# Performance work log

Hardware: AMD Instinct MI355X
Metric: run time of the kernel (lower is better)

## Reference

```python
import jax, jax.numpy as jnp
import numpy as np

B, N, IN, HID, OUT = 64, 256, 7, 64, 32
DEG = 32
NT = B * N          # total nodes per side
E = NT * DEG        # intra-graph edges per side
TAU = 1.0
MAX_ITER = 10
EPS = 1e-5          # InstanceNorm2d eps


def setup_inputs() -> dict:
    key = jax.random.key(0)
    ks = jax.random.split(key, 12)

    def edges(k):
        # random intra-graph edges: local indices in [0, N) plus per-graph offset
        loc = jax.random.randint(k, (2, B, N * DEG), 0, N)
        off = (jnp.arange(B) * N)[None, :, None]
        return (loc + off).reshape(2, -1).astype(jnp.int64)

    def lin(k, fi, fo):
        return jax.random.normal(k, (fi, fo), jnp.float32) / np.float32(np.sqrt(fi))

    return {
        "x1": jax.random.normal(ks[0], (NT, IN), jnp.float32),
        "x2": jax.random.normal(ks[1], (NT, IN), jnp.float32),
        "edge1": edges(ks[2]),
        "edge2": edges(ks[3]),
        "Wl1": lin(ks[4], IN, HID), "Wr1": lin(ks[5], IN, HID),
        "bl1": jnp.zeros((HID,), jnp.float32), "br1": jnp.zeros((HID,), jnp.float32),
        "att1": jax.random.normal(ks[6], (HID,), jnp.float32) * 0.1,
        "bias1": jnp.zeros((HID,), jnp.float32),
        "Wl2": lin(ks[7], HID, OUT), "Wr2": lin(ks[8], HID, OUT),
        "bl2": jnp.zeros((OUT,), jnp.float32), "br2": jnp.zeros((OUT,), jnp.float32),
        "att2": jax.random.normal(ks[9], (OUT,), jnp.float32) * 0.1,
        "bias2": jnp.zeros((OUT,), jnp.float32),
        "gamma": jnp.ones((1,), jnp.float32),
        "beta": jnp.zeros((1,), jnp.float32),
    }


def _gatv2(x, src, dst, Wl, bl, Wr, br, att, bias):
    # PyG GATv2Conv, heads=1: score = att . leaky_relu(lin_l(x_j) + lin_r(x_i))
    xl = x @ Wl + bl  # source transform
    xr = x @ Wr + br  # target transform
    e = jax.nn.leaky_relu(xl[src] + xr[dst], 0.2)     # [E, D]
    score = e @ att                                    # [E]
    smax = jax.ops.segment_max(score, dst, num_segments=NT)
    ex = jnp.exp(score - smax[dst])
    den = jax.ops.segment_sum(ex, dst, num_segments=NT)
    alpha = ex / den[dst]
    out = jax.ops.segment_sum(alpha[:, None] * xl[src], dst, num_segments=NT)
    return out + bias


def _encode(x, edge, params):
    # add self loops (PyG add_self_loops=True default)
    loops = jnp.arange(NT)
    src = jnp.concatenate([edge[0], loops])
    dst = jnp.concatenate([edge[1], loops])
    h = jax.nn.relu(_gatv2(x, src, dst, *params[0]))
    return _gatv2(h, src, dst, *params[1])


def _soft_topk(sim_n):
    # AFAT-style differentiable top-k: OT between flattened scores and
    # {min, max} anchors with marginals [(n-k)/n, k/n], k = N2 per pair.
    n = N * N
    k = N
    flat = sim_n.reshape(B, n)
    mn = flat.min(axis=1, keepdims=True)
    mx = flat.max(axis=1, keepdims=True)
    dist = jnp.stack([flat - mn, mx - flat], axis=-1)  # [B, n, 2] (|s-min|,|s-max|)
    logK = -dist / TAU
    log_row = -jnp.log(jnp.float32(n))
    log_col = jnp.log(jnp.array([(n - k) / n, k / n], jnp.float32))
    for i in range(MAX_ITER):
        if i % 2 == 0:  # row normalization to uniform 1/n
            logK = logK - jax.scipy.special.logsumexp(logK, axis=-1, keepdims=True) + log_row
        else:           # column normalization to [(n-k)/n, k/n]
            logK = logK - jax.scipy.special.logsumexp(logK, axis=1, keepdims=True) + log_col[None, None, :]
    soft = jnp.clip(jnp.exp(logK[:, :, 1]) * n, 0.0, 1.0)  # selection probability per entry
    return soft.reshape(B, N, N)


def reference(x1, x2, edge1, edge2, Wl1, Wr1, bl1, br1, att1, bias1,
              Wl2, Wr2, bl2, br2, att2, bias2, gamma, beta):
    params = ((Wl1, bl1, Wr1, br1, att1, bias1), (Wl2, bl2, Wr2, br2, att2, bias2))
    h1 = _encode(x1, edge1, params).reshape(B, N, OUT)
    h2 = _encode(x2, edge2, params).reshape(B, N, OUT)
    sim = jnp.einsum('bnd,bmd->bnm', h1, h2)
    # InstanceNorm2d(1, affine=True): normalize each pair's sim matrix
    mu = sim.mean(axis=(1, 2), keepdims=True)
    var = sim.var(axis=(1, 2), keepdims=True)
    sim_n = gamma[0] * (sim - mu) * jax.lax.rsqrt(var + EPS) + beta[0]
    return _soft_topk(sim_n)  # soft_S stacked over the batch, [B, N, N]
```

## Files before the change

### kernel.cpp

```cpp
#include <hip/hip_runtime.h>

#define NB 64
#define NN 256
#define IND 7
#define HIDD 64
#define OUTD 32
#define EPG 8192
#define ETOT 524288
#define CAPQ 2600
#define SRCPAD 2624

typedef _Float16 f16;
typedef f16 f16x2 __attribute__((ext_vector_type(2)));
typedef f16 f16x4 __attribute__((ext_vector_type(4)));
typedef f16 f16x8 __attribute__((ext_vector_type(8)));
typedef float f32x4 __attribute__((ext_vector_type(4)));

__device__ __forceinline__ float bsum16(float v, float* rb){
#pragma unroll
  for (int o = 32; o > 0; o >>= 1) v += __shfl_xor(v, o, 64);
  __syncthreads();
  if ((threadIdx.x & 63) == 0) rb[threadIdx.x >> 6] = v;
  __syncthreads();
  float s = 0.f;
#pragma unroll
  for (int i = 0; i < 16; i++) s += rb[i];
  return s;
}

__device__ __forceinline__ f16x2 lrelu2(f16x2 s){
  const f16x2 k = {(f16)0.2f, (f16)0.2f};
  return __builtin_elementwise_max(s, s * k);
}

__global__ __launch_bounds__(512, 4) void gat1(
    const float* __restrict__ x1, const float* __restrict__ x2,
    const int* __restrict__ e1, const int* __restrict__ e2,
    const float* __restrict__ Wl, const float* __restrict__ Wr,
    const float* __restrict__ bl, const float* __restrict__ br,
    const float* __restrict__ att, const float* __restrict__ bias,
    const float* __restrict__ Wl2, const float* __restrict__ Wr2,
    const float* __restrict__ bl2, const float* __restrict__ br2,
    f16* __restrict__ xl2, f16* __restrict__ xr2,
    int* __restrict__ meta, unsigned char* __restrict__ srcs)
{
  __shared__ __align__(16) f16 xl_s[256 * 72];
  __shared__ __align__(16) f16 xr1_s[64 * 72];
  __shared__ __align__(16) f16 att_s[64];
  __shared__ float sc_s[CAPQ + 8];
  __shared__ unsigned int src_su[SRCPAD / 4];
  __shared__ int deg_s[64], start_s[64], cnt_s[64];
  __shared__ unsigned char perm[64];
  unsigned char* src_s = (unsigned char*)src_su;

  const int bid = blockIdx.x;
  const int gs = bid & 127, lo = (bid >> 7) * 64;
  const int side = gs >> 6, g = gs & 63;
  const float* x = side ? x2 : x1;
  const int* eb = side ? e2 : e1;
  const int* es = eb + g * EPG;
  const int* ed = eb + ETOT + g * EPG;
  const int t = threadIdx.x;
  const int wv = t >> 6, lane64 = t & 63;

  if (t < 64){ deg_s[t] = 0; att_s[t] = (f16)att[t]; }

  unsigned int ep2[9];
  int nE = 0;
#pragma unroll
  for (int i = 0; i < 17; i++){
    int e = t + i * 512;
    if (e < EPG + 256){
      int sl, dl;
      if (e < EPG){ sl = es[e] & 255; dl = ed[e] & 255; }
      else { sl = dl = e - EPG; }
      unsigned int pk = (unsigned int)((dl << 8) | sl);
      if ((i & 1) == 0) ep2[i >> 1] = pk;
      else ep2[i >> 1] |= pk << 16;
      nE = i + 1;
    }
  }

  float xvl[IND], xvr[IND];
  {
    const int nodel = (wv & 3) * 64 + lane64;
    const float* pl = x + (g * 256 + nodel) * IND;
    const float* pr = x + (g * 256 + lo + lane64) * IND;
#pragma unroll
    for (int k = 0; k < IND; k++){ xvl[k] = pl[k]; xvr[k] = pr[k]; }
  }
  __syncthreads();

#pragma unroll
  for (int i = 0; i < 17; i++) if (i < nE){
    unsigned int pk = (ep2[i >> 1] >> (16 * (i & 1))) & 0xFFFFu;
    int r = (int)(pk >> 8) - lo;
    if ((unsigned)r < 64u) atomicAdd(&deg_s[r], 1);
  }
  __syncthreads();
  if (t < 64){
    int v = deg_s[t], s = v;
#pragma unroll
    for (int off = 1; off < 64; off <<= 1){
      int u = __shfl_up(s, off, 64);
      if (t >= off) s += u;
    }
    start_s[t] = s - v;
    cnt_s[t] = s - v;
    meta[bid * 128 + t] = s - v;
    meta[bid * 128 + 64 + t] = v;
    int r = 0;
#pragma unroll 8
    for (int j = 0; j < 64; j++){
      int dj = deg_s[j];
      r += (dj < v) || (dj == v && j < t);
    }
    perm[r] = (unsigned char)t;
  }
  __syncthreads();
#pragma unroll
  for (int i = 0; i < 17; i++) if (i < nE){
    unsigned int pk = (ep2[i >> 1] >> (16 * (i & 1))) & 0xFFFFu;
    int r = (int)(pk >> 8) - lo;
    if ((unsigned)r < 64u){
      int p = atomicAdd(&cnt_s[r], 1);
      if (p < CAPQ) src_s[p] = (unsigned char)(pk & 255u);
    }
  }
  __syncthreads();
  {
    int ttl = start_s[63] + deg_s[63];
    if (ttl > CAPQ) ttl = CAPQ;
    unsigned int* gsrc = (unsigned int*)(srcs + (size_t)bid * SRCPAD);
    int nw = (ttl + 3) >> 2;
    for (int i = t; i < nw; i += 512) gsrc[i] = src_su[i];
  }

  {
    const int ng = wv & 3, dh = wv >> 2;
    const int node = ng * 64 + lane64;
#pragma unroll
    for (int ch = 0; ch < 4; ch++){
      const int d0 = dh * 32 + ch * 8;
      float a[8];
#pragma unroll
      for (int d = 0; d < 8; d++) a[d] = bl[d0 + d];
#pragma unroll
      for (int k = 0; k < IND; k++){
        float xk = xvl[k];
#pragma unroll
        for (int d = 0; d < 8; d++)
          a[d] = fmaf(xk, Wl[k * HIDD + d0 + d], a[d]);
      }
      f16x8 o;
#pragma unroll
      for (int j = 0; j < 8; j++) o[j] = (f16)a[j];
      *(f16x8*)&xl_s[node * 72 + d0] = o;
    }
  }
  {
    const int d0 = wv * 8;
    float a[8];
#pragma unroll
    for (int d = 0; d < 8; d++) a[d] = br[d0 + d];
#pragma unroll
    for (int k = 0; k < IND; k++){
      float xk = xvr[k];
#pragma unroll
      for (int d = 0; d < 8; d++)
        a[d] = fmaf(xk, Wr[k * HIDD + d0 + d], a[d]);
    }
    f16x8 o;
#pragma unroll
    for (int j = 0; j < 8; j++) o[j] = (f16)a[j];
    *(f16x8*)&xr1_s[lane64 * 72 + d0] = o;
  }
  __syncthreads();

  const int pairi = perm[t >> 3], sub = t & 7, ln = lo + pairi;
  f16x2 xrh[32], atth[32];
  {
    const f16x8* xrp = (const f16x8*)&xr1_s[pairi * 72];
    const f16x8* atp = (const f16x8*)att_s;
#pragma unroll
    for (int q = 0; q < 8; q++){
      f16x8 v = xrp[q], a_ = atp[q];
#pragma unroll
      for (int u = 0; u < 4; u++){
        xrh[q * 4 + u][0] = v[2 * u];
        xrh[q * 4 + u][1] = v[2 * u + 1];
        atth[q * 4 + u][0] = a_[2 * u];
        atth[q * 4 + u][1] = a_[2 * u + 1];
      }
    }
  }

  const int s0 = start_s[pairi];
  int sE = s0 + deg_s[pairi];
  if (sE > CAPQ) sE = CAPQ;
  float ssum = 0.f;
  for (int idx = s0 + sub; idx < sE; idx += 8){
    int sl = src_s[idx];
    const f16x8* rp = (const f16x8*)&xl_s[(unsigned)sl * 72];
    float accs[4] = {0.f, 0.f, 0.f, 0.f};
#pragma unroll
    for (int blk = 0; blk < 8; blk++){
      f16x8 rv = rp[blk];
#pragma unroll
      for (int u = 0; u < 4; u++){
        f16x2 v = {rv[2 * u], rv[2 * u + 1]};
        v = v + xrh[blk * 4 + u];
        accs[u] = __builtin_amdgcn_fdot2(lrelu2(v), atth[blk * 4 + u], accs[u], false);
      }
    }
    float w = __expf((accs[0] + accs[1]) + (accs[2] + accs[3]));
    sc_s[idx] = w;
    ssum += w;
  }
  ssum += __shfl_xor(ssum, 1, 64);
  ssum += __shfl_xor(ssum, 2, 64);
  ssum += __shfl_xor(ssum, 4, 64);
  float inv = 1.f / ssum;
  float acc[8];
#pragma unroll
  for (int c = 0; c < 8; c++) acc[c] = 0.f;
  for (int base = s0; base < sE; base += 4){
    f16x8 rows[4]; float wv_[4];
#pragma unroll
    for (int k = 0; k < 4; k++){
      int sl = src_s[base + k];
      rows[k] = *(const f16x8*)&xl_s[(unsigned)sl * 72 + sub * 8];
      wv_[k] = sc_s[base + k];
    }
#pragma unroll
    for (int k = 0; k < 4; k++){
      float w = (base + k < sE) ? wv_[k] : 0.f;
#pragma unroll
      for (int c = 0; c < 8; c++) acc[c] = fmaf(w, (float)rows[k][c], acc[c]);
    }
  }
  f16x8 o;
#pragma unroll
  for (int c = 0; c < 8; c++)
    o[c] = (f16)fmaxf(acc[c] * inv + bias[sub * 8 + c], 0.f);

  __syncthreads();
  *(f16x8*)&xl_s[pairi * 72 + sub * 8] = o;
  __syncthreads();
  if (wv < 4){
    const int m = lane64 & 15, quad = lane64 >> 4;
    const int row = wv * 16 + m;
    f16x8 a0 = *(const f16x8*)&xl_s[row * 72 + quad * 8];
    f16x8 a1 = *(const f16x8*)&xl_s[row * 72 + 32 + quad * 8];
#pragma unroll
    for (int mat = 0; mat < 2; mat++){
      const float* W = mat ? Wr2 : Wl2;
      const float* bb = mat ? br2 : bl2;
      f16* dst = mat ? xr2 : xl2;
#pragma unroll
      for (int H = 0; H < 2; H++){
        const int n = H * 16 + m;
        f16x8 b0, b1;
#pragma unroll
        for (int j = 0; j < 8; j++){
          b0[j] = (f16)W[(quad * 8 + j) * 32 + n];
          b1[j] = (f16)W[(32 + quad * 8 + j) * 32 + n];
        }
        const float bv = bb[n];
        f32x4 accm = {0.f, 0.f, 0.f, 0.f};
        accm = __builtin_amdgcn_mfma_f32_16x16x32_f16(a0, b0, accm, 0, 0, 0);
        accm = __builtin_amdgcn_mfma_f32_16x16x32_f16(a1, b1, accm, 0, 0, 0);
#pragma unroll
        for (int r = 0; r < 4; r++)
          dst[(size_t)(gs * 256 + lo + wv * 16 + quad * 4 + r) * 32 + n]
              = (f16)(accm[r] + bv);
      }
    }
  }
}

__global__ __launch_bounds__(512, 4) void gat2(
    const int* __restrict__ meta, const unsigned char* __restrict__ srcs,
    const f16* __restrict__ xl2, const f16* __restrict__ xr2,
    const float* __restrict__ att, const float* __restrict__ bias,
    f16* __restrict__ hout)
{
  __shared__ __align__(16) f16 xl_s[256 * 40];
  __shared__ __align__(16) f16 xr_s[64 * 40];
  __shared__ float sc_s[CAPQ + 8];
  __shared__ unsigned int src_su[SRCPAD / 4];
  __shared__ int start_s[64], deg_s[64];
  __shared__ unsigned char perm[64];
  unsigned char* src_s = (unsigned char*)src_su;

  const int bid = blockIdx.x;
  const int gs = bid & 127, lo = (bid >> 7) * 64;
  const int t = threadIdx.x;

  if (t < 64){
    start_s[t] = meta[bid * 128 + t];
    deg_s[t] = meta[bid * 128 + 64 + t];
  }
  {
    int ttl = meta[bid * 128 + 63] + meta[bid * 128 + 64 + 63];
    if (ttl > CAPQ) ttl = CAPQ;
    const unsigned int* gsrc = (const unsigned int*)(srcs + (size_t)bid * SRCPAD);
    int nw = (ttl + 3) >> 2;
    for (int i = t; i < nw; i += 512) src_su[i] = gsrc[i];
  }

  {
    const int row = t >> 1, half = t & 1;
    const f16* s_ = xl2 + (size_t)(gs * 256 + row) * 32 + half * 16;
    *(f16x8*)&xl_s[row * 40 + half * 16] = *(const f16x8*)s_;
    *(f16x8*)&xl_s[row * 40 + half * 16 + 8] = *(const f16x8*)(s_ + 8);
    if (t < 128){
      const f16* s2_ = xr2 + (size_t)(gs * 256 + lo + row) * 32 + half * 16;
      *(f16x8*)&xr_s[row * 40 + half * 16] = *(const f16x8*)s2_;
      *(f16x8*)&xr_s[row * 40 + half * 16 + 8] = *(const f16x8*)(s2_ + 8);
    }
  }
  __syncthreads();
  if (t < 64){
    int v = deg_s[t], r = 0;
#pragma unroll 8
    for (int j = 0; j < 64; j++){
      int dj = deg_s[j];
      r += (dj < v) || (dj == v && j < t);
    }
    perm[r] = (unsigned char)t;
  }
  __syncthreads();

  const int pairi = perm[t >> 3], sub = t & 7, ln = lo + pairi;
  f16x2 xrh[16], atth[16];
  {
    const f16x8* xrp = (const f16x8*)&xr_s[pairi * 40];
#pragma unroll
    for (int q = 0; q < 4; q++){
      f16x8 v = xrp[q];
#pragma unroll
      for (int u = 0; u < 4; u++){
        xrh[q * 4 + u][0] = v[2 * u];
        xrh[q * 4 + u][1] = v[2 * u + 1];
      }
    }
#pragma unroll
    for (int i = 0; i < 16; i++){
      atth[i][0] = (f16)att[2 * i];
      atth[i][1] = (f16)att[2 * i + 1];
    }
  }

  const int s0 = start_s[pairi];
  int sE = s0 + deg_s[pairi];
  if (sE > CAPQ) sE = CAPQ;
  float ssum = 0.f;
  for (int idx = s0 + sub; idx < sE; idx += 8){
    int sl = src_s[idx];
    const f16x8* rp = (const f16x8*)&xl_s[(unsigned)sl * 40];
    float accs[4] = {0.f, 0.f, 0.f, 0.f};
#pragma unroll
    for (int blk = 0; blk < 4; blk++){
      f16x8 rv = rp[blk];
#pragma unroll
      for (int u = 0; u < 4; u++){
        f16x2 v = {rv[2 * u], rv[2 * u + 1]};
        v = v + xrh[blk * 4 + u];
        accs[u] = __builtin_amdgcn_fdot2(lrelu2(v), atth[blk * 4 + u], accs[u], false);
      }
    }
    float w = __expf((accs[0] + accs[1]) + (accs[2] + accs[3]));
    sc_s[idx] = w;
    ssum += w;
  }
  ssum += __shfl_xor(ssum, 1, 64);
  ssum += __shfl_xor(ssum, 2, 64);
  ssum += __shfl_xor(ssum, 4, 64);
  float inv = 1.f / ssum;

  float acc[4];
#pragma unroll
  for (int c = 0; c < 4; c++) acc[c] = 0.f;
  for (int base = s0; base < sE; base += 8){
    f16x4 rows[8]; float wv[8];
#pragma unroll
    for (int k = 0; k < 8; k++){
      int sl = src_s[base + k];
      rows[k] = *(const f16x4*)&xl_s[(unsigned)sl * 40 + sub * 4];
      wv[k] = sc_s[base + k];
    }
#pragma unroll
    for (int k = 0; k < 8; k++){
      float w = (base + k < sE) ? wv[k] : 0.f;
#pragma unroll
      for (int c = 0; c < 4; c++) acc[c] = fmaf(w, (float)rows[k][c], acc[c]);
    }
  }
  f16x4 o;
#pragma unroll
  for (int c = 0; c < 4; c++)
    o[c] = (f16)(acc[c] * inv + bias[sub * 4 + c]);
  *(f16x4*)(hout + (size_t)(gs * 256 + ln) * 32 + sub * 4) = o;
}

__global__ __launch_bounds__(1024) void sinkout(
    const f16* __restrict__ H,
    const float* __restrict__ gamma, const float* __restrict__ beta,
    float* __restrict__ out)
{
  __shared__ float rb[16];
  __shared__ __align__(16) float rb4s[64];
  __shared__ unsigned int hist[8192];
  const int b = blockIdx.x & 63, q = blockIdx.x >> 6, t = threadIdx.x;
  const int w = t >> 6, lane = t & 63;
  const int m = lane & 15, quad = lane >> 4;

  const f16* h1 = H + (size_t)b * 256 * 32;
  const f16* h2 = H + (size_t)(64 + b) * 256 * 32;

  f16x8 av = *(const f16x8*)(h1 + (size_t)(w * 16 + m) * 32 + quad * 8);
  f32x4 c[16];
#pragma unroll
  for (int j = 0; j < 16; j++){
    f16x8 bv = *(const f16x8*)(h2 + (size_t)(j * 16 + m) * 32 + quad * 8);
    f32x4 z = {0.f, 0.f, 0.f, 0.f};
    c[j] = __builtin_amdgcn_mfma_f32_16x16x32_f16(av, bv, z, 0, 0, 0);
  }

  float sm = 0.f, s2 = 0.f, mn = 3.0e38f, mx = -3.0e38f;
#pragma unroll
  for (int j = 0; j < 16; j++)
#pragma unroll
    for (int r = 0; r < 4; r++){
      float s = c[j][r];
      sm += s; s2 = fmaf(s, s, s2);
      mn = fminf(mn, s); mx = fmaxf(mx, s);
    }
#pragma unroll
  for (int o = 32; o > 0; o >>= 1){
    sm += __shfl_xor(sm, o, 64);
    s2 += __shfl_xor(s2, o, 64);
    mn = fminf(mn, __shfl_xor(mn, o, 64));
    mx = fmaxf(mx, __shfl_xor(mx, o, 64));
  }
  if (lane == 0){
    rb4s[w * 4 + 0] = sm; rb4s[w * 4 + 1] = s2;
    rb4s[w * 4 + 2] = mn; rb4s[w * 4 + 3] = mx;
  }
  for (int i = t; i < 8192; i += 1024) hist[i] = 0u;
  __syncthreads();
  sm = 0.f; s2 = 0.f; mn = 3.0e38f; mx = -3.0e38f;
#pragma unroll
  for (int i = 0; i < 16; i++){
    sm += rb4s[i * 4 + 0];
    s2 += rb4s[i * 4 + 1];
    mn = fminf(mn, rb4s[i * 4 + 2]);
    mx = fmaxf(mx, rb4s[i * 4 + 3]);
  }

  const float mu = sm * (1.f / 65536.f);
  const float var = s2 * (1.f / 65536.f) - mu * mu;
  const float a = gamma[0] * rsqrtf(var + 1e-5f);
  const float cc = beta[0] - a * mu;
  float mnn = a * mn + cc, mxn = a * mx + cc;
  if (a < 0.f){ float tmp = mnn; mnn = mxn; mxn = tmp; }
  const float al = 2.f * a;
  const float be = 2.f * cc - mnn - mxn;
  const float R = fmaxf(mxn - mnn, 1e-12f);
  const float binscale = 4096.f / R;

#pragma unroll
  for (int j = 0; j < 16; j++)
#pragma unroll
    for (int r = 0; r < 4; r++){
      float z = fmaf(al, c[j][r], be);
      int bi = (int)fmaf(z, binscale, 4096.f);
      bi = min(max(bi, 0), 8191);
      atomicAdd(&hist[bi], 1u);
    }
  __syncthreads();

  const float wbin = R * (1.f / 4096.f);
  float ebs[8], cnts[8];
#pragma unroll
  for (int j = 0; j < 8; j++){
    float zc = fmaf((float)(t * 8 + j) + 0.5f, wbin, -R);
    ebs[j] = __expf(-zc);
    cnts[j] = (float)hist[t * 8 + j];
  }

  float D = 0.f, S = 256.f, eD = 1.f;
  for (int p = 0; p < 5; p++){
    float loc = 0.f;
#pragma unroll
    for (int j = 0; j < 8; j++)
      loc += cnts[j] / (1.f + ebs[j] * eD);
    S = bsum16(loc, rb);
    if (p < 4){
      D += -5.5412635f  + __logf(65536.f - S) - __logf(S);
      eD = __expf(-D);
    }
  }

  const float beD = be + D;
  const float scale = 256.f / S;
  if ((w >> 2) == q){
    float* ob = out + (size_t)b * 65536;
#pragma unroll
    for (int j = 0; j < 16; j++){
#pragma unroll
      for (int r = 0; r < 4; r++){
        float zz = fmaf(al, c[j][r], beD);
        float v = fminf(scale / (1.f + __expf(-zz)), 1.f);
        ob[(w * 16 + quad * 4 + r) * 256 + j * 16 + m] = v;
      }
    }
  }
}

extern "C" void kernel_launch(void* const* d_in, const int* in_sizes, int n_in,
                              void* d_out, int out_size, void* d_ws, size_t ws_size,
                              hipStream_t stream)
{
  const float* x1   = (const float*)d_in[0];
  const float* x2   = (const float*)d_in[1];
  const int*   e1   = (const int*)d_in[2];
  const int*   e2   = (const int*)d_in[3];
  const float* Wl1  = (const float*)d_in[4];
  const float* Wr1  = (const float*)d_in[5];
  const float* bl1  = (const float*)d_in[6];
  const float* br1  = (const float*)d_in[7];
  const float* att1 = (const float*)d_in[8];
  const float* bias1= (const float*)d_in[9];
  const float* Wl2  = (const float*)d_in[10];
  const float* Wr2  = (const float*)d_in[11];
  const float* bl2  = (const float*)d_in[12];
  const float* br2  = (const float*)d_in[13];
  const float* att2 = (const float*)d_in[14];
  const float* bias2= (const float*)d_in[15];
  const float* gamma= (const float*)d_in[16];
  const float* beta = (const float*)d_in[17];

  char* ws = (char*)d_ws;
  f16* hfin = (f16*)ws;
  f16* xl2 = (f16*)(ws + (size_t)2 * 1024 * 1024);
  f16* xr2 = (f16*)(ws + (size_t)4 * 1024 * 1024);
  int* meta = (int*)(ws + (size_t)6 * 1024 * 1024);
  unsigned char* srcs = (unsigned char*)(ws + (size_t)6 * 1024 * 1024 + 512 * 128 * 4);
  float* out = (float*)d_out;

  gat1<<<512, 512, 0, stream>>>(x1, x2, e1, e2, Wl1, Wr1, bl1, br1, att1, bias1,
                                Wl2, Wr2, bl2, br2, xl2, xr2, meta, srcs);
  gat2<<<512, 512, 0, stream>>>(meta, srcs, xl2, xr2, att2, bias2, hfin);
  sinkout<<<256, 1024, 0, stream>>>(hfin, gamma, beta, out);
}
```

Before: 160.9 us.

## Fuse GAT attention scoring into aggregation pass with cross-lane dot reduction

Both GAT kernels drop the separate scoring pass that had each thread read whole source rows, compute scores and store exp weights to shared memory. Each thread now computes a partial attention dot product over its own 8- or 4-feature slice of the rows it already loads for aggregation. The partials are combined with xor shuffles across the 8-lane group, and the softmax denominator is accumulated in the same loop. This removes one full pass of shared-memory row reads, the sc_s buffer and a large per-thread register array, at the cost of three shuffles per edge and redundant exp evaluation in every lane.

```diff
diff --git a/kernel.cpp b/kernel.cpp
--- a/kernel.cpp
+++ b/kernel.cpp
@@ -47,7 +47,6 @@
   __shared__ __align__(16) f16 xl_s[256 * 72];
   __shared__ __align__(16) f16 xr1_s[64 * 72];
   __shared__ __align__(16) f16 att_s[64];
-  __shared__ float sc_s[CAPQ + 8];
   __shared__ unsigned int src_su[SRCPAD / 4];
   __shared__ int deg_s[64], start_s[64], cnt_s[64];
   __shared__ unsigned char perm[64];
@@ -178,20 +177,14 @@
   __syncthreads();
 
   const int pairi = perm[t >> 3], sub = t & 7, ln = lo + pairi;
-  f16x2 xrh[32], atth[32];
-  {
-    const f16x8* xrp = (const f16x8*)&xr1_s[pairi * 72];
-    const f16x8* atp = (const f16x8*)att_s;
-#pragma unroll
-    for (int q = 0; q < 8; q++){
-      f16x8 v = xrp[q], a_ = atp[q];
-#pragma unroll
-      for (int u = 0; u < 4; u++){
-        xrh[q * 4 + u][0] = v[2 * u];
-        xrh[q * 4 + u][1] = v[2 * u + 1];
-        atth[q * 4 + u][0] = a_[2 * u];
-        atth[q * 4 + u][1] = a_[2 * u + 1];
-      }
+  f16x2 xr4[4], at4[4];
+  {
+    f16x8 v = *(const f16x8*)&xr1_s[pairi * 72 + sub * 8];
+    f16x8 a_ = *(const f16x8*)&att_s[sub * 8];
+#pragma unroll
+    for (int u = 0; u < 4; u++){
+      xr4[u][0] = v[2 * u];  xr4[u][1] = v[2 * u + 1];
+      at4[u][0] = a_[2 * u]; at4[u][1] = a_[2 * u + 1];
     }
   }
 
@@ -199,46 +192,40 @@
   int sE = s0 + deg_s[pairi];
   if (sE > CAPQ) sE = CAPQ;
   float ssum = 0.f;
-  for (int idx = s0 + sub; idx < sE; idx += 8){
-    int sl = src_s[idx];
-    const f16x8* rp = (const f16x8*)&xl_s[(unsigned)sl * 72];
-    float accs[4] = {0.f, 0.f, 0.f, 0.f};
-#pragma unroll
-    for (int blk = 0; blk < 8; blk++){
-      f16x8 rv = rp[blk];
-#pragma unroll
-      for (int u = 0; u < 4; u++){
-        f16x2 v = {rv[2 * u], rv[2 * u + 1]};
-        v = v + xrh[blk * 4 + u];
-        accs[u] = __builtin_amdgcn_fdot2(lrelu2(v), atth[blk * 4 + u], accs[u], false);
-      }
-    }
-    float w = __expf((accs[0] + accs[1]) + (accs[2] + accs[3]));
-    sc_s[idx] = w;
-    ssum += w;
-  }
-  ssum += __shfl_xor(ssum, 1, 64);
-  ssum += __shfl_xor(ssum, 2, 64);
-  ssum += __shfl_xor(ssum, 4, 64);
-  float inv = 1.f / ssum;
   float acc[8];
 #pragma unroll
   for (int c = 0; c < 8; c++) acc[c] = 0.f;
   for (int base = s0; base < sE; base += 4){
-    f16x8 rows[4]; float wv_[4];
+    f16x8 rows[4];
 #pragma unroll
     for (int k = 0; k < 4; k++){
       int sl = src_s[base + k];
       rows[k] = *(const f16x8*)&xl_s[(unsigned)sl * 72 + sub * 8];
-      wv_[k] = sc_s[base + k];
-    }
+    }
+    float w4[4];
 #pragma unroll
     for (int k = 0; k < 4; k++){
-      float w = (base + k < sE) ? wv_[k] : 0.f;
+      float p = 0.f;
+#pragma unroll
+      for (int u = 0; u < 4; u++){
+        f16x2 v = {rows[k][2 * u], rows[k][2 * u + 1]};
+        v = v + xr4[u];
+        p = __builtin_amdgcn_fdot2(lrelu2(v), at4[u], p, false);
+      }
+      p += __shfl_xor(p, 1, 64);
+      p += __shfl_xor(p, 2, 64);
+      p += __shfl_xor(p, 4, 64);
+      w4[k] = __expf(p);
+    }
+#pragma unroll
+    for (int k = 0; k < 4; k++){
+      float w = (base + k < sE) ? w4[k] : 0.f;
+      ssum += w;
 #pragma unroll
       for (int c = 0; c < 8; c++) acc[c] = fmaf(w, (float)rows[k][c], acc[c]);
     }
   }
+  float inv = 1.f / ssum;
   f16x8 o;
 #pragma unroll
   for (int c = 0; c < 8; c++)
@@ -287,7 +274,6 @@
 {
   __shared__ __align__(16) f16 xl_s[256 * 40];
   __shared__ __align__(16) f16 xr_s[64 * 40];
-  __shared__ float sc_s[CAPQ + 8];
   __shared__ unsigned int src_su[SRCPAD / 4];
   __shared__ int start_s[64], deg_s[64];
   __shared__ unsigned char perm[64];
@@ -333,70 +319,52 @@
   __syncthreads();
 
   const int pairi = perm[t >> 3], sub = t & 7, ln = lo + pairi;
-  f16x2 xrh[16], atth[16];
-  {
-    const f16x8* xrp = (const f16x8*)&xr_s[pairi * 40];
-#pragma unroll
-    for (int q = 0; q < 4; q++){
-      f16x8 v = xrp[q];
-#pragma unroll
-      for (int u = 0; u < 4; u++){
-        xrh[q * 4 + u][0] = v[2 * u];
-        xrh[q * 4 + u][1] = v[2 * u + 1];
-      }
-    }
-#pragma unroll
-    for (int i = 0; i < 16; i++){
-      atth[i][0] = (f16)att[2 * i];
-      atth[i][1] = (f16)att[2 * i + 1];
-    }
+  f16x2 xr2f[2], at2f[2];
+  {
+    f16x4 v = *(const f16x4*)&xr_s[pairi * 40 + sub * 4];
+    xr2f[0][0] = v[0]; xr2f[0][1] = v[1];
+    xr2f[1][0] = v[2]; xr2f[1][1] = v[3];
+    at2f[0][0] = (f16)att[sub * 4 + 0]; at2f[0][1] = (f16)att[sub * 4 + 1];
+    at2f[1][0] = (f16)att[sub * 4 + 2]; at2f[1][1] = (f16)att[sub * 4 + 3];
   }
 
   const int s0 = start_s[pairi];
   int sE = s0 + deg_s[pairi];
   if (sE > CAPQ) sE = CAPQ;
   float ssum = 0.f;
-  for (int idx = s0 + sub; idx < sE; idx += 8){
-    int sl = src_s[idx];
-    const f16x8* rp = (const f16x8*)&xl_s[(unsigned)sl * 40];
-    float accs[4] = {0.f, 0.f, 0.f, 0.f};
-#pragma unroll
-    for (int blk = 0; blk < 4; blk++){
-      f16x8 rv = rp[blk];
-#pragma unroll
-      for (int u = 0; u < 4; u++){
-        f16x2 v = {rv[2 * u], rv[2 * u + 1]};
-        v = v + xrh[blk * 4 + u];
-        accs[u] = __builtin_amdgcn_fdot2(lrelu2(v), atth[blk * 4 + u], accs[u], false);
-      }
-    }
-    float w = __expf((accs[0] + accs[1]) + (accs[2] + accs[3]));
-    sc_s[idx] = w;
-    ssum += w;
-  }
-  ssum += __shfl_xor(ssum, 1, 64);
-  ssum += __shfl_xor(ssum, 2, 64);
-  ssum += __shfl_xor(ssum, 4, 64);
-  float inv = 1.f / ssum;
-
   float acc[4];
 #pragma unroll
   for (int c = 0; c < 4; c++) acc[c] = 0.f;
   for (int base = s0; base < sE; base += 8){
-    f16x4 rows[8]; float wv[8];
+    f16x4 rows[8];
 #pragma unroll
     for (int k = 0; k < 8; k++){
       int sl = src_s[base + k];
       rows[k] = *(const f16x4*)&xl_s[(unsigned)sl * 40 + sub * 4];
-      wv[k] = sc_s[base + k];
-    }
+    }
+    float w8[8];
 #pragma unroll
     for (int k = 0; k < 8; k++){
-      float w = (base + k < sE) ? wv[k] : 0.f;
+      f16x2 v0 = {rows[k][0], rows[k][1]};
+      f16x2 v1 = {rows[k][2], rows[k][3]};
+      v0 = v0 + xr2f[0];
+      v1 = v1 + xr2f[1];
+      float p = __builtin_amdgcn_fdot2(lrelu2(v0), at2f[0], 0.f, false);
+      p = __builtin_amdgcn_fdot2(lrelu2(v1), at2f[1], p, false);
+      p += __shfl_xor(p, 1, 64);
+      p += __shfl_xor(p, 2, 64);
+      p += __shfl_xor(p, 4, 64);
+      w8[k] = __expf(p);
+    }
+#pragma unroll
+    for (int k = 0; k < 8; k++){
+      float w = (base + k < sE) ? w8[k] : 0.f;
+      ssum += w;
 #pragma unroll
       for (int c = 0; c < 4; c++) acc[c] = fmaf(w, (float)rows[k][c], acc[c]);
     }
   }
+  float inv = 1.f / ssum;
   f16x4 o;
 #pragma unroll
   for (int c = 0; c < 4; c++)
```

New measurement: 164.9 us. 2.4% more time.
